# Kernel tuning notes

Hardware: AMD Instinct MI355X
Metric: run time of the kernel (lower is better)

Reference implementation:

```python
import jax, jax.numpy as jnp
import numpy as np

B, L = 8, 2048          # images, lines per image
C_IN, HW = 256, 128     # backbone feature channels, spatial size
DIM_LOI = 128
N_PTS0, N_PTS1 = 32, 8  # sampled points per line, after maxpool
SCALE = N_PTS0 // N_PTS1
EPS = 1e-5


def setup_inputs() -> dict:
    key = jax.random.key(0)
    ks = jax.random.split(key, 24)
    d = {}
    d['feature'] = jax.random.normal(ks[0], (B, C_IN, HW, HW), jnp.float32)
    # line endpoints in pixel coords [0, 128)
    d['lines'] = jax.random.uniform(ks[1], (B, L, 2, 2), jnp.float32) * HW
    # fc1: 1x1 conv 256 -> 128
    d['fc1_w'] = jax.random.normal(ks[2], (DIM_LOI, C_IN), jnp.float32) * 0.05
    d['fc1_b'] = jnp.zeros((DIM_LOI,), jnp.float32)
    planes = DIM_LOI // 2
    def bn(k, c):
        k1, k2, k3 = jax.random.split(k, 3)
        return (jax.random.normal(k1, (c,), jnp.float32) * 0.1 + 1.0,
                jax.random.normal(k2, (c,), jnp.float32) * 0.1,
                jax.random.normal(k3, (c,), jnp.float32) * 0.05,
                jax.random.uniform(jax.random.fold_in(k, 7), (c,), jnp.float32, 0.5, 1.5))
    d['bn1_g'], d['bn1_b'], d['bn1_m'], d['bn1_v'] = bn(ks[3], DIM_LOI)
    d['conv1_w'] = jax.random.normal(ks[4], (planes, DIM_LOI), jnp.float32) * 0.05
    d['conv1_b'] = jnp.zeros((planes,), jnp.float32)
    d['bn2_g'], d['bn2_b'], d['bn2_m'], d['bn2_v'] = bn(ks[5], planes)
    d['conv2_w'] = jax.random.normal(ks[6], (planes, planes, 3), jnp.float32) * 0.05
    d['conv2_b'] = jnp.zeros((planes,), jnp.float32)
    d['bn3_g'], d['bn3_b'], d['bn3_m'], d['bn3_v'] = bn(ks[7], planes)
    d['conv3_w'] = jax.random.normal(ks[8], (DIM_LOI, planes), jnp.float32) * 0.05
    d['conv3_b'] = jnp.zeros((DIM_LOI,), jnp.float32)
    d['fc2_w'] = jax.random.normal(ks[9], (1, DIM_LOI * N_PTS1), jnp.float32) * 0.02
    d['fc2_b'] = jnp.zeros((1,), jnp.float32)
    return d


def _bn(x, g, b, m, v):
    # x: [N, C, T], eval-mode batchnorm
    s = g * jax.lax.rsqrt(v + EPS)
    return x * s[None, :, None] + (b - m * s)[None, :, None]


def _loi_forward(feature, lines, fc1_w, fc1_b,
                 bn1_g, bn1_b, bn1_m, bn1_v, conv1_w, conv1_b,
                 bn2_g, bn2_b, bn2_m, bn2_v, conv2_w, conv2_b,
                 bn3_g, bn3_b, bn3_m, bn3_v, conv3_w, conv3_b,
                 fc2_w, fc2_b):
    # fc1: 1x1 conv -> [B, DIM_LOI, H, W]
    x = jnp.einsum('oc,bchw->bohw', fc1_w, feature) + fc1_b[None, :, None, None]

    # sample N_PTS0 points per line: p = p0*lam + p1*(1-lam) - 0.5
    lam = jnp.linspace(0.0, 1.0, N_PTS0, dtype=lines.dtype)  # [P]
    pts = (lines[:, :, 0, None, :] * lam[None, None, :, None]
           + lines[:, :, 1, None, :] * (1.0 - lam[None, None, :, None]) - 0.5)  # [B,L,P,2]
    px, py = pts[..., 0], pts[..., 1]
    px0 = jnp.clip(jnp.floor(px), 0.0, HW - 1.0)
    py0 = jnp.clip(jnp.floor(py), 0.0, HW - 1.0)
    px1 = jnp.clip(px0 + 1.0, 0.0, HW - 1.0)
    py1 = jnp.clip(py0 + 1.0, 0.0, HW - 1.0)
    px0l, py0l = px0.astype(jnp.int32), py0.astype(jnp.int32)
    px1l, py1l = px1.astype(jnp.int32), py1.astype(jnp.int32)

    def gather(f, ix, iy):  # f: [C,H,W], ix/iy: [L,P] -> [C,L,P]
        return f[:, ix, iy]

    gat = jax.vmap(gather)  # over batch
    xp = (gat(x, px0l, py0l) * ((px1 - px) * (py1 - py))[:, None]
          + gat(x, px1l, py0l) * ((px - px0) * (py1 - py))[:, None]
          + gat(x, px0l, py1l) * ((px1 - px) * (py - py0))[:, None]
          + gat(x, px1l, py1l) * ((px - px0) * (py - py0))[:, None])  # [B,C,L,P]

    xp = xp.transpose(0, 2, 1, 3).reshape(B * L, DIM_LOI, N_PTS0)  # [N,C,P]
    # MaxPool1d(kernel=stride=SCALE)
    xp = xp.reshape(B * L, DIM_LOI, N_PTS1, SCALE).max(axis=-1)  # [N,C,T=8]

    # Bottleneck1D residual: x + op(x)
    h = jax.nn.relu(_bn(xp, bn1_g, bn1_b, bn1_m, bn1_v))
    h = jnp.einsum('oc,nct->not', conv1_w, h) + conv1_b[None, :, None]
    h = jax.nn.relu(_bn(h, bn2_g, bn2_b, bn2_m, bn2_v))
    h = jax.lax.conv_general_dilated(h, conv2_w, (1,), [(1, 1)],
                                     dimension_numbers=('NCH', 'OIH', 'NCH'))
    h = h + conv2_b[None, :, None]
    h = jax.nn.relu(_bn(h, bn3_g, bn3_b, bn3_m, bn3_v))
    h = jnp.einsum('oc,nct->not', conv3_w, h) + conv3_b[None, :, None]
    xp = xp + h

    # fc2: ReLU -> Linear(dim_loi*n_pts1, 1)
    flat = jax.nn.relu(xp).reshape(B * L, DIM_LOI * N_PTS1)
    logits = (flat @ fc2_w.T + fc2_b).reshape(-1)  # [B*L]
    return logits


def reference(feature, lines, fc1_w, fc1_b,
              bn1_g, bn1_b, bn1_m, bn1_v, conv1_w, conv1_b,
              bn2_g, bn2_b, bn2_m, bn2_v, conv2_w, conv2_b,
              bn3_g, bn3_b, bn3_m, bn3_v, conv3_w, conv3_b,
              fc2_w, fc2_b):
    return _loi_forward(feature, lines, fc1_w, fc1_b,
                        bn1_g, bn1_b, bn1_m, bn1_v, conv1_w, conv1_b,
                        bn2_g, bn2_b, bn2_m, bn2_v, conv2_w, conv2_b,
                        bn3_g, bn3_b, bn3_m, bn3_v, conv3_w, conv3_b,
                        fc2_w, fc2_b)
```

## Files before the change

### kernel.cpp

```cpp
#include <hip/hip_runtime.h>

#define EPSBN 1e-5f

typedef _Float16 f16;
typedef _Float16 f16x8 __attribute__((ext_vector_type(8)));
typedef _Float16 f16x4 __attribute__((ext_vector_type(4)));
typedef _Float16 f16x2 __attribute__((ext_vector_type(2)));
typedef float    f32x4 __attribute__((ext_vector_type(4)));

__device__ inline unsigned int pack2(float a, float b) {
    union { f16x2 h; unsigned int u; } cv;
    cv.h[0] = (f16)a; cv.h[1] = (f16)b;
    return cv.u;
}
__device__ inline f16x4 hmax4(f16x4 a, f16x4 b) {
    f16x4 r;
    #pragma unroll
    for (int i = 0; i < 4; ++i) r[i] = a[i] > b[i] ? a[i] : b[i];
    return r;
}
__device__ inline f16x8 relu8(f16x8 v) {
    f16x8 r;
    #pragma unroll
    for (int i = 0; i < 8; ++i) r[i] = v[i] > (f16)0.f ? v[i] : (f16)0.f;
    return r;
}

__global__ void wprep_kernel(const float* __restrict__ fc1w,
                             const float* __restrict__ w1,
                             const float* __restrict__ w2,
                             const float* __restrict__ w3,
                             f16* __restrict__ dst) {
    const int i = blockIdx.x * 256 + threadIdx.x;
    float v;
    if (i < 32768)      v = fc1w[i];
    else if (i < 40960) v = w1[i - 32768];
    else if (i < 53248) {
        const int j = i - 40960, tau = j >> 12, rest = j & 4095;
        v = w2[rest * 3 + tau];
    } else              v = w3[i - 53248];
    dst[i] = (f16)v;
}

__global__ __launch_bounds__(256, 4)
void fc1_mfma(const float* __restrict__ feat,
              const f16*   __restrict__ w16,
              const float* __restrict__ bias,
              f16*         __restrict__ xmap) {
    __shared__ unsigned int ldsu[64 * 130];

    const int tid  = threadIdx.x;
    const int wv   = tid >> 6, lane = tid & 63;
    const int n16  = lane & 15, quad = lane >> 4;
    const int b    = blockIdx.x & 7;
    const int p0   = (blockIdx.x >> 3) * 64;
    const int lane16 = tid & 15;
    const int r2     = tid >> 4;

    const float* fbase = feat + ((size_t)b << 22) + p0 + lane16 * 4;
    #pragma unroll
    for (int i = 0; i < 8; ++i) {
        const int kp = r2 + 16 * i;
        const float* ra = fbase + ((size_t)(2 * kp) << 14);
        const float4 f4a = *(const float4*)ra;
        const float4 f4b = *(const float4*)(ra + 16384);
        ldsu[(lane16 * 4 + 0) * 130 + kp] = pack2(f4a.x, f4b.x);
        ldsu[(lane16 * 4 + 1) * 130 + kp] = pack2(f4a.y, f4b.y);
        ldsu[(lane16 * 4 + 2) * 130 + kp] = pack2(f4a.z, f4b.z);
        ldsu[(lane16 * 4 + 3) * 130 + kp] = pack2(f4a.w, f4b.w);
    }
    __syncthreads();

    f32x4 acc[8];
    #pragma unroll
    for (int nt = 0; nt < 8; ++nt) acc[nt] = (f32x4){0.f, 0.f, 0.f, 0.f};

    const unsigned int* arow = ldsu + (wv * 16 + n16) * 130;
    #pragma unroll
    for (int ks = 0; ks < 8; ++ks) {
        const int c = ks * 16 + quad * 4;
        union { f16x8 v; f16x4 h[2]; } af;
        af.h[0] = *(const f16x4*)&arow[c];
        af.h[1] = *(const f16x4*)&arow[c + 2];
        #pragma unroll
        for (int nt = 0; nt < 8; ++nt) {
            const f16x8 bf = *(const f16x8*)&w16[(size_t)(nt * 16 + n16) * 256
                                                 + ks * 32 + quad * 8];
            acc[nt] = __builtin_amdgcn_mfma_f32_16x16x32_f16(af.v, bf, acc[nt], 0, 0, 0);
        }
    }
    __syncthreads();

    f16* ep = (f16*)ldsu;
    #pragma unroll
    for (int nt = 0; nt < 8; ++nt) {
        const int o = nt * 16 + n16;
        const float bo = bias[o];
        #pragma unroll
        for (int r = 0; r < 4; ++r)
            ep[(wv * 16 + quad * 4 + r) * 136 + o] = (f16)(acc[nt][r] + bo);
    }
    __syncthreads();

    #pragma unroll
    for (int it = 0; it < 4; ++it) {
        const int u = tid + 256 * it;
        const int row = u >> 4, cg = u & 15;
        const float4 v = *(const float4*)&ep[row * 136 + cg * 8];
        *(float4*)&xmap[(((size_t)((b << 14) + p0 + row)) << 7) + cg * 8] = v;
    }
}

__global__ __launch_bounds__(256)
void loi_kernel(const f16*   __restrict__ x,
                const float* __restrict__ lines,
                const f16*   __restrict__ wsp,
                const float* __restrict__ bn1g, const float* __restrict__ bn1b,
                const float* __restrict__ bn1m, const float* __restrict__ bn1v,
                const float* __restrict__ b1,
                const float* __restrict__ bn2g, const float* __restrict__ bn2b,
                const float* __restrict__ bn2m, const float* __restrict__ bn2v,
                const float* __restrict__ b2,
                const float* __restrict__ bn3g, const float* __restrict__ bn3b,
                const float* __restrict__ bn3m, const float* __restrict__ bn3v,
                const float* __restrict__ b3,
                const float* __restrict__ fc2w, const float* __restrict__ fc2b,
                float* __restrict__ out) {
    __shared__ f16 xp[64][136];
    __shared__ alignas(16) union {
        struct { int toff[256][4]; f16 twgt[256][4]; } tp;
        struct { f16 h1[80][72]; f16 h2[64][72]; } cv;
    } u;
    __shared__ f16 s1h[128], t1h[128];
    __shared__ float s2f[64], t2f[64], s3f[64], t3f[64], b1f[64], b2f[64];
    __shared__ float b3f[128];
    __shared__ float wsum[4][8];

    const f16* w1f16 = wsp + 32768;
    const f16* w2f16 = wsp + 40960;
    const f16* w3f16 = wsp + 53248;

    const int tid  = threadIdx.x;
    const int wv   = tid >> 6, lane = tid & 63;
    const int n16  = lane & 15, quad = lane >> 4;
    const int img  = blockIdx.x & 7;
    const int mblk = blockIdx.x >> 3;

    if (tid < 128) {
        const float s = bn1g[tid] * rsqrtf(bn1v[tid] + EPSBN);
        s1h[tid] = (f16)s; t1h[tid] = (f16)(bn1b[tid] - bn1m[tid] * s);
    }
    if (tid < 64) {
        const float s = bn2g[tid] * rsqrtf(bn2v[tid] + EPSBN);
        s2f[tid] = s; t2f[tid] = bn2b[tid] - bn2m[tid] * s;
        b1f[tid] = b1[tid];
    } else if (tid < 128) {
        const int c = tid - 64;
        const float s = bn3g[c] * rsqrtf(bn3v[c] + EPSBN);
        s3f[c] = s; t3f[c] = bn3b[c] - bn3m[c] * s;
        b2f[c] = b2[c];
    } else {
        b3f[tid - 128] = b3[tid - 128];
    }

    {
        const int li = tid >> 5, pt = tid & 31;
        const int gl = img * 2048 + mblk * 8 + li;
        const float4 ln = *(const float4*)&lines[gl * 4];
        const float lam = (float)pt * (1.0f / 31.0f);
        const float px = ln.x * lam + ln.z * (1.f - lam) - 0.5f;
        const float py = ln.y * lam + ln.w * (1.f - lam) - 0.5f;
        const float px0 = fminf(fmaxf(floorf(px), 0.f), 127.f);
        const float py0 = fminf(fmaxf(floorf(py), 0.f), 127.f);
        const float px1 = fminf(px0 + 1.f, 127.f);
        const float py1 = fminf(py0 + 1.f, 127.f);
        const int ix0 = (int)px0, iy0 = (int)py0;
        const int ix1 = (int)px1, iy1 = (int)py1;
        u.tp.toff[tid][0] = (((ix0 << 7) + iy0) << 7);
        u.tp.toff[tid][1] = (((ix1 << 7) + iy0) << 7);
        u.tp.toff[tid][2] = (((ix0 << 7) + iy1) << 7);
        u.tp.toff[tid][3] = (((ix1 << 7) + iy1) << 7);
        const float wx1 = px1 - px, wx0 = px - px0;
        const float wy1 = py1 - py, wy0 = py - py0;
        u.tp.twgt[tid][0] = (f16)(wx1 * wy1); u.tp.twgt[tid][1] = (f16)(wx0 * wy1);
        u.tp.twgt[tid][2] = (f16)(wx1 * wy0); u.tp.twgt[tid][3] = (f16)(wx0 * wy0);
    }
    __syncthreads();

    {
        const int h = lane >> 5, j = lane & 31;
        const int li = wv * 2 + h;
        const f16* xbh = x + (((size_t)img) << 21) + 4 * j;
        #pragma unroll
        for (int t = 0; t < 8; ++t) {
            f16x4 m = {(f16)(-60000.f), (f16)(-60000.f), (f16)(-60000.f), (f16)(-60000.f)};
            #pragma unroll
            for (int s = 0; s < 4; ++s) {
                const int combo = li * 32 + t * 4 + s;
                const int4  off = *(const int4*)&u.tp.toff[combo][0];
                const f16x4 tw  = *(const f16x4*)&u.tp.twgt[combo][0];
                const f16x4 g00 = *(const f16x4*)(xbh + off.x);
                const f16x4 g10 = *(const f16x4*)(xbh + off.y);
                const f16x4 g01 = *(const f16x4*)(xbh + off.z);
                const f16x4 g11 = *(const f16x4*)(xbh + off.w);
                const f16x4 w0 = {tw[0], tw[0], tw[0], tw[0]};
                const f16x4 w1v = {tw[1], tw[1], tw[1], tw[1]};
                const f16x4 w2v = {tw[2], tw[2], tw[2], tw[2]};
                const f16x4 w3v = {tw[3], tw[3], tw[3], tw[3]};
                f16x4 v = g00 * w0 + g10 * w1v + g01 * w2v + g11 * w3v;
                m = hmax4(m, v);
            }
            *(f16x4*)&xp[li * 8 + t][4 * j] = m;
        }
    }
    __syncthreads();

    {
        const int r = tid >> 4, seg = tid & 15;
        const int row = (r >> 1) * 10 + (r & 1) * 9;
        *(unsigned long long*)&u.cv.h1[row][seg * 4] = 0ull;
    }

    {
        const int o_lane = wv * 16 + n16;
        f32x4 acc1[4];
        #pragma unroll
        for (int nt = 0; nt < 4; ++nt) acc1[nt] = (f32x4){0.f, 0.f, 0.f, 0.f};
        #pragma unroll
        for (int ks = 0; ks < 4; ++ks) {
            const int k = ks * 32 + quad * 8;
            const f16x8 a  = *(const f16x8*)&w1f16[o_lane * 128 + k];
            const f16x8 s8 = *(const f16x8*)&s1h[k];
            const f16x8 t8 = *(const f16x8*)&t1h[k];
            #pragma unroll
            for (int nt = 0; nt < 4; ++nt) {
                const f16x8 raw = *(const f16x8*)&xp[nt * 16 + n16][k];
                const f16x8 bf = relu8(raw * s8 + t8);
                acc1[nt] = __builtin_amdgcn_mfma_f32_16x16x32_f16(a, bf, acc1[nt], 0, 0, 0);
            }
        }
        #pragma unroll
        for (int nt = 0; nt < 4; ++nt) {
            const int n = nt * 16 + n16;
            const int nprow = (n >> 3) * 10 + (n & 7) + 1;
            #pragma unroll
            for (int r = 0; r < 4; ++r) {
                const int o = wv * 16 + quad * 4 + r;
                const float v = fmaxf((acc1[nt][r] + b1f[o]) * s2f[o] + t2f[o], 0.f);
                u.cv.h1[nprow][o] = (f16)v;
            }
        }
    }
    __syncthreads();

    {
        const int o_lane = wv * 16 + n16;
        f32x4 acc2[4];
        #pragma unroll
        for (int nt = 0; nt < 4; ++nt) acc2[nt] = (f32x4){0.f, 0.f, 0.f, 0.f};
        #pragma unroll
        for (int d = 0; d < 3; ++d) {
            const f16* A2 = w2f16 + d * 4096;
            #pragma unroll
            for (int ks = 0; ks < 2; ++ks) {
                const int k = ks * 32 + quad * 8;
                const f16x8 a = *(const f16x8*)&A2[o_lane * 64 + k];
                #pragma unroll
                for (int nt = 0; nt < 4; ++nt) {
                    const int n = nt * 16 + n16;
                    const int row = (n >> 3) * 10 + (n & 7) + d;
                    const f16x8 bf = *(const f16x8*)&u.cv.h1[row][k];
                    acc2[nt] = __builtin_amdgcn_mfma_f32_16x16x32_f16(a, bf, acc2[nt], 0, 0, 0);
                }
            }
        }
        #pragma unroll
        for (int nt = 0; nt < 4; ++nt) {
            const int n = nt * 16 + n16;
            #pragma unroll
            for (int r = 0; r < 4; ++r) {
                const int o = wv * 16 + quad * 4 + r;
                const float v = fmaxf((acc2[nt][r] + b2f[o]) * s3f[o] + t3f[o], 0.f);
                u.cv.h2[n][o] = (f16)v;
            }
        }
    }
    __syncthreads();

    {
        const int col = n16 & 7, obase = wv * 16 + quad * 4;
        float fcv[2][4];
        #pragma unroll
        for (int h = 0; h < 2; ++h)
            #pragma unroll
            for (int r = 0; r < 4; ++r)
                fcv[h][r] = fc2w[(h * 64 + obase + r) * 8 + col];

        f32x4 acc3[2][4];
        #pragma unroll
        for (int h = 0; h < 2; ++h)
            #pragma unroll
            for (int nt = 0; nt < 4; ++nt) acc3[h][nt] = (f32x4){0.f, 0.f, 0.f, 0.f};
        #pragma unroll
        for (int ks = 0; ks < 2; ++ks) {
            const int k = ks * 32 + quad * 8;
            const f16x8 a0 = *(const f16x8*)&w3f16[(wv * 16 + n16) * 64 + k];
            const f16x8 a1 = *(const f16x8*)&w3f16[(64 + wv * 16 + n16) * 64 + k];
            #pragma unroll
            for (int nt = 0; nt < 4; ++nt) {
                const f16x8 bf = *(const f16x8*)&u.cv.h2[nt * 16 + n16][k];
                acc3[0][nt] = __builtin_amdgcn_mfma_f32_16x16x32_f16(a0, bf, acc3[0][nt], 0, 0, 0);
                acc3[1][nt] = __builtin_amdgcn_mfma_f32_16x16x32_f16(a1, bf, acc3[1][nt], 0, 0, 0);
            }
        }
        float part[4] = {0.f, 0.f, 0.f, 0.f};
        #pragma unroll
        for (int h = 0; h < 2; ++h) {
            const float4 bq = *(const float4*)&b3f[h * 64 + obase];
            const float bqa[4] = {bq.x, bq.y, bq.z, bq.w};
            #pragma unroll
            for (int nt = 0; nt < 4; ++nt) {
                const int n = nt * 16 + n16;
                const f16x4 rx = *(const f16x4*)&xp[n][h * 64 + obase];
                float p = 0.f;
                #pragma unroll
                for (int r = 0; r < 4; ++r) {
                    float v = acc3[h][nt][r] + bqa[r] + (float)rx[r];
                    v = fmaxf(v, 0.f);
                    p += v * fcv[h][r];
                }
                part[nt] += p;
            }
        }
        #pragma unroll
        for (int off_i = 0; off_i < 5; ++off_i) {
            const int off = (int[]){1, 2, 4, 16, 32}[off_i];
            part[0] += __shfl_xor(part[0], off, 64);
            part[1] += __shfl_xor(part[1], off, 64);
            part[2] += __shfl_xor(part[2], off, 64);
            part[3] += __shfl_xor(part[3], off, 64);
        }
        if ((lane & 55) == 0) {
            const int par = (lane >> 3) & 1;
            wsum[wv][0 + par] = part[0];
            wsum[wv][2 + par] = part[1];
            wsum[wv][4 + par] = part[2];
            wsum[wv][6 + par] = part[3];
        }
    }
    __syncthreads();

    if (tid < 8) {
        const float s = wsum[0][tid] + wsum[1][tid] + wsum[2][tid] + wsum[3][tid];
        out[img * 2048 + mblk * 8 + tid] = s + fc2b[0];
    }
}

extern "C" void kernel_launch(void* const* d_in, const int* in_sizes, int n_in,
                              void* d_out, int out_size, void* d_ws, size_t ws_size,
                              hipStream_t stream) {
    const float* feature = (const float*)d_in[0];
    const float* lines   = (const float*)d_in[1];
    const float* fc1_w   = (const float*)d_in[2];
    const float* fc1_b   = (const float*)d_in[3];
    const float* bn1g    = (const float*)d_in[4];
    const float* bn1b    = (const float*)d_in[5];
    const float* bn1m    = (const float*)d_in[6];
    const float* bn1v    = (const float*)d_in[7];
    const float* w1      = (const float*)d_in[8];
    const float* b1      = (const float*)d_in[9];
    const float* bn2g    = (const float*)d_in[10];
    const float* bn2b    = (const float*)d_in[11];
    const float* bn2m    = (const float*)d_in[12];
    const float* bn2v    = (const float*)d_in[13];
    const float* w2      = (const float*)d_in[14];
    const float* b2      = (const float*)d_in[15];
    const float* bn3g    = (const float*)d_in[16];
    const float* bn3b    = (const float*)d_in[17];
    const float* bn3m    = (const float*)d_in[18];
    const float* bn3v    = (const float*)d_in[19];
    const float* w3      = (const float*)d_in[20];
    const float* b3      = (const float*)d_in[21];
    const float* fc2w    = (const float*)d_in[22];
    const float* fc2b    = (const float*)d_in[23];

    f16* xmap = (f16*)d_ws;
    f16* wsp  = (f16*)((char*)d_ws + (size_t)32 * 1024 * 1024);

    wprep_kernel<<<240, 256, 0, stream>>>(fc1_w, w1, w2, w3, wsp);
    fc1_mfma<<<2048, 256, 0, stream>>>(feature, wsp, fc1_b, xmap);
    loi_kernel<<<2048, 256, 0, stream>>>(xmap, lines, wsp,
                                         bn1g, bn1b, bn1m, bn1v, b1,
                                         bn2g, bn2b, bn2m, bn2v, b2,
                                         bn3g, bn3b, bn3m, bn3v, b3,
                                         fc2w, fc2b, (float*)d_out);
}
```

Measured before the change: 340.2 us.

## Split fc1 into fp16 transpose pass and tiled MFMA GEMM, chunked by image pairs

Replaces the fused fc1 kernel, which read fp32 NCHW features and transposed them in LDS, with two kernels. The first converts features to a pixel-major fp16 layout. The second is a 128x128-tile MFMA GEMM with register prefetch of the next K chunk. Work runs in four chunks of two images so the intermediate stays small and may stay cache-resident. This adds an extra write and read of the transposed features and eight more launches, in exchange for coalesced loads and more reuse of the weights.

Result: slower. 362.0 us (+6.4%).

```diff
diff --git a/kernel.cpp b/kernel.cpp
--- a/kernel.cpp
+++ b/kernel.cpp
@@ -8,11 +8,6 @@
 typedef _Float16 f16x2 __attribute__((ext_vector_type(2)));
 typedef float    f32x4 __attribute__((ext_vector_type(4)));
 
-__device__ inline unsigned int pack2(float a, float b) {
-    union { f16x2 h; unsigned int u; } cv;
-    cv.h[0] = (f16)a; cv.h[1] = (f16)b;
-    return cv.u;
-}
 __device__ inline f16x4 hmax4(f16x4 a, f16x4 b) {
     f16x4 r;
     #pragma unroll
@@ -42,72 +37,119 @@
     dst[i] = (f16)v;
 }
 
-__global__ __launch_bounds__(256, 4)
-void fc1_mfma(const float* __restrict__ feat,
-              const f16*   __restrict__ w16,
-              const float* __restrict__ bias,
-              f16*         __restrict__ xmap) {
-    __shared__ unsigned int ldsu[64 * 130];
+__global__ __launch_bounds__(256)
+void transpose_kernel(const float* __restrict__ feat,
+                      f16* __restrict__ featT,
+                      int b0) {
+    __shared__ float lds[64][129];
+
+    const int tid = threadIdx.x, wv = tid >> 6, lane = tid & 63;
+    const int bq  = blockIdx.x & 1;
+    const int kc  = (blockIdx.x >> 1) & 3;
+    const int p0  = (blockIdx.x >> 3) * 128;
+    const int k0  = kc * 64;
+
+    const float* src = feat + ((size_t)(b0 + bq) << 22) + (size_t)k0 * 16384 + p0;
+
+    #pragma unroll
+    for (int j = 0; j < 8; ++j) {
+        const int row = wv * 16 + 2 * j + (lane >> 5);
+        const int col = (lane & 31) * 4;
+        const float4 v = *(const float4*)(src + (size_t)row * 16384 + col);
+        *(float4*)&lds[row][col] = v;
+    }
+    __syncthreads();
+
+    const int a = lane >> 3, b = lane & 7;
+    #pragma unroll
+    for (int it = 0; it < 4; ++it) {
+        const int p = 8 * wv + a + 32 * it;
+        f16x8 h;
+        #pragma unroll
+        for (int j = 0; j < 8; ++j) h[j] = (f16)lds[b * 8 + j][p];
+        *(f16x8*)&featT[(((size_t)bq << 14) + p0 + p) * 256 + k0 + b * 8] = h;
+    }
+}
+
+__global__ __launch_bounds__(256)
+void gemm_kernel(const f16*   __restrict__ featT,
+                 const f16*   __restrict__ w16,
+                 const float* __restrict__ bias,
+                 f16*         __restrict__ xmap,
+                 int b0) {
+    __shared__ union {
+        f16 A[128][72];
+        f16 E[128][136];
+    } u;
 
     const int tid  = threadIdx.x;
     const int wv   = tid >> 6, lane = tid & 63;
     const int n16  = lane & 15, quad = lane >> 4;
-    const int b    = blockIdx.x & 7;
-    const int p0   = (blockIdx.x >> 3) * 64;
-    const int lane16 = tid & 15;
-    const int r2     = tid >> 4;
-
-    const float* fbase = feat + ((size_t)b << 22) + p0 + lane16 * 4;
-    #pragma unroll
-    for (int i = 0; i < 8; ++i) {
-        const int kp = r2 + 16 * i;
-        const float* ra = fbase + ((size_t)(2 * kp) << 14);
-        const float4 f4a = *(const float4*)ra;
-        const float4 f4b = *(const float4*)(ra + 16384);
-        ldsu[(lane16 * 4 + 0) * 130 + kp] = pack2(f4a.x, f4b.x);
-        ldsu[(lane16 * 4 + 1) * 130 + kp] = pack2(f4a.y, f4b.y);
-        ldsu[(lane16 * 4 + 2) * 130 + kp] = pack2(f4a.z, f4b.z);
-        ldsu[(lane16 * 4 + 3) * 130 + kp] = pack2(f4a.w, f4b.w);
-    }
-    __syncthreads();
-
-    f32x4 acc[8];
-    #pragma unroll
-    for (int nt = 0; nt < 8; ++nt) acc[nt] = (f32x4){0.f, 0.f, 0.f, 0.f};
-
-    const unsigned int* arow = ldsu + (wv * 16 + n16) * 130;
-    #pragma unroll
-    for (int ks = 0; ks < 8; ++ks) {
-        const int c = ks * 16 + quad * 4;
-        union { f16x8 v; f16x4 h[2]; } af;
-        af.h[0] = *(const f16x4*)&arow[c];
-        af.h[1] = *(const f16x4*)&arow[c + 2];
+    const int bq   = blockIdx.x & 1;
+    const int p0   = (blockIdx.x >> 1) * 128;
+    const int seg  = lane & 7;
+    const int rowb = wv * 8 + (lane >> 3);
+
+    const f16* src = featT + (((size_t)bq << 14) + p0) * 256;
+
+    f32x4 acc[2][8];
+    #pragma unroll
+    for (int mt = 0; mt < 2; ++mt)
+        #pragma unroll
+        for (int nt = 0; nt < 8; ++nt) acc[mt][nt] = (f32x4){0.f, 0.f, 0.f, 0.f};
+
+    f16x8 pf[4];
+    #pragma unroll
+    for (int it = 0; it < 4; ++it)
+        pf[it] = *(const f16x8*)(src + (size_t)(rowb + 32 * it) * 256 + seg * 8);
+
+    for (int kc = 0; kc < 4; ++kc) {
+        #pragma unroll
+        for (int it = 0; it < 4; ++it)
+            *(f16x8*)&u.A[rowb + 32 * it][seg * 8] = pf[it];
+        __syncthreads();
+        if (kc < 3) {
+            #pragma unroll
+            for (int it = 0; it < 4; ++it)
+                pf[it] = *(const f16x8*)(src + (size_t)(rowb + 32 * it) * 256
+                                         + (kc + 1) * 64 + seg * 8);
+        }
+        #pragma unroll
+        for (int s = 0; s < 2; ++s) {
+            const int kl = s * 32 + quad * 8;
+            const f16x8 a0 = *(const f16x8*)&u.A[(2 * wv + 0) * 16 + n16][kl];
+            const f16x8 a1 = *(const f16x8*)&u.A[(2 * wv + 1) * 16 + n16][kl];
+            #pragma unroll
+            for (int nt = 0; nt < 8; ++nt) {
+                const f16x8 bf = *(const f16x8*)&w16[(size_t)(nt * 16 + n16) * 256
+                                                     + kc * 64 + kl];
+                acc[0][nt] = __builtin_amdgcn_mfma_f32_16x16x32_f16(a0, bf, acc[0][nt], 0, 0, 0);
+                acc[1][nt] = __builtin_amdgcn_mfma_f32_16x16x32_f16(a1, bf, acc[1][nt], 0, 0, 0);
+            }
+        }
+        __syncthreads();
+    }
+
+    #pragma unroll
+    for (int mt = 0; mt < 2; ++mt) {
         #pragma unroll
         for (int nt = 0; nt < 8; ++nt) {
-            const f16x8 bf = *(const f16x8*)&w16[(size_t)(nt * 16 + n16) * 256
-                                                 + ks * 32 + quad * 8];
-            acc[nt] = __builtin_amdgcn_mfma_f32_16x16x32_f16(af.v, bf, acc[nt], 0, 0, 0);
-        }
-    }
-    __syncthreads();
-
-    f16* ep = (f16*)ldsu;
-    #pragma unroll
-    for (int nt = 0; nt < 8; ++nt) {
-        const int o = nt * 16 + n16;
-        const float bo = bias[o];
-        #pragma unroll
-        for (int r = 0; r < 4; ++r)
-            ep[(wv * 16 + quad * 4 + r) * 136 + o] = (f16)(acc[nt][r] + bo);
-    }
-    __syncthreads();
-
-    #pragma unroll
-    for (int it = 0; it < 4; ++it) {
-        const int u = tid + 256 * it;
-        const int row = u >> 4, cg = u & 15;
-        const float4 v = *(const float4*)&ep[row * 136 + cg * 8];
-        *(float4*)&xmap[(((size_t)((b << 14) + p0 + row)) << 7) + cg * 8] = v;
+            const int o = nt * 16 + n16;
+            const float bo = bias[o];
+            #pragma unroll
+            for (int r = 0; r < 4; ++r)
+                u.E[(2 * wv + mt) * 16 + quad * 4 + r][o] = (f16)(acc[mt][nt][r] + bo);
+        }
+    }
+    __syncthreads();
+
+    const int bglob = b0 + bq;
+    #pragma unroll
+    for (int it = 0; it < 8; ++it) {
+        const int uu = tid + 256 * it;
+        const int row = uu >> 4, cg = uu & 15;
+        const float4 v = *(const float4*)&u.E[row][cg * 8];
+        *(float4*)&xmap[(((size_t)((bglob << 14) + p0 + row)) << 7) + cg * 8] = v;
     }
 }
 
@@ -384,11 +426,17 @@
     const float* fc2w    = (const float*)d_in[22];
     const float* fc2b    = (const float*)d_in[23];
 
-    f16* xmap = (f16*)d_ws;
-    f16* wsp  = (f16*)((char*)d_ws + (size_t)32 * 1024 * 1024);
+    f16* wsp   = (f16*)d_ws;
+    f16* xmap  = (f16*)((char*)d_ws + (size_t)131072);
+    f16* featT = (f16*)((char*)d_ws + (size_t)131072 + (size_t)32 * 1024 * 1024);
 
     wprep_kernel<<<240, 256, 0, stream>>>(fc1_w, w1, w2, w3, wsp);
-    fc1_mfma<<<2048, 256, 0, stream>>>(feature, wsp, fc1_b, xmap);
+
+    for (int b0 = 0; b0 < 8; b0 += 2) {
+        transpose_kernel<<<1024, 256, 0, stream>>>(feature, featT, b0);
+        gemm_kernel<<<256, 256, 0, stream>>>(featT, wsp, fc1_b, xmap, b0);
+    }
+
     loi_kernel<<<2048, 256, 0, stream>>>(xmap, lines, wsp,
                                          bn1g, bn1b, bn1m, bn1v, b1,
                                          bn2g, bn2b, bn2m, bn2v, b2,
```

## Pipeline fc1 feature loads in K-chunks with register prefetch and smaller LDS

Applied to the files above, without the earlier changes.

The fc1 GEMM kernel now streams the 256 input channels in four chunks of 64. It stages fp32 tiles in a smaller LDS buffer and prefetches the next chunk into registers while MFMAs run on the current one, instead of loading all channels up front as packed fp16. This is meant to overlap global loads with compute and cut LDS footprint for higher occupancy. The fp16 conversion moves to the LDS read side, and the launch-bounds occupancy hint is dropped. The workspace layout is also swapped so the weights come first and xmap follows at a small offset.

New measurement: 355.8 us. +4.6%, slower.

```diff
diff --git a/kernel.cpp b/kernel.cpp
--- a/kernel.cpp
+++ b/kernel.cpp
@@ -8,11 +8,6 @@
 typedef _Float16 f16x2 __attribute__((ext_vector_type(2)));
 typedef float    f32x4 __attribute__((ext_vector_type(4)));
 
-__device__ inline unsigned int pack2(float a, float b) {
-    union { f16x2 h; unsigned int u; } cv;
-    cv.h[0] = (f16)a; cv.h[1] = (f16)b;
-    return cv.u;
-}
 __device__ inline f16x4 hmax4(f16x4 a, f16x4 b) {
     f16x4 r;
     #pragma unroll
@@ -42,71 +37,80 @@
     dst[i] = (f16)v;
 }
 
-__global__ __launch_bounds__(256, 4)
+__global__ __launch_bounds__(256)
 void fc1_mfma(const float* __restrict__ feat,
               const f16*   __restrict__ w16,
               const float* __restrict__ bias,
               f16*         __restrict__ xmap) {
-    __shared__ unsigned int ldsu[64 * 130];
+    __shared__ union {
+        float A[64][66];
+        f16   E[64][136];
+    } u;
 
     const int tid  = threadIdx.x;
     const int wv   = tid >> 6, lane = tid & 63;
     const int n16  = lane & 15, quad = lane >> 4;
     const int b    = blockIdx.x & 7;
     const int p0   = (blockIdx.x >> 3) * 64;
-    const int lane16 = tid & 15;
-    const int r2     = tid >> 4;
-
-    const float* fbase = feat + ((size_t)b << 22) + p0 + lane16 * 4;
-    #pragma unroll
-    for (int i = 0; i < 8; ++i) {
-        const int kp = r2 + 16 * i;
-        const float* ra = fbase + ((size_t)(2 * kp) << 14);
-        const float4 f4a = *(const float4*)ra;
-        const float4 f4b = *(const float4*)(ra + 16384);
-        ldsu[(lane16 * 4 + 0) * 130 + kp] = pack2(f4a.x, f4b.x);
-        ldsu[(lane16 * 4 + 1) * 130 + kp] = pack2(f4a.y, f4b.y);
-        ldsu[(lane16 * 4 + 2) * 130 + kp] = pack2(f4a.z, f4b.z);
-        ldsu[(lane16 * 4 + 3) * 130 + kp] = pack2(f4a.w, f4b.w);
-    }
-    __syncthreads();
+    const int krow = tid >> 4;
+    const int pcol = (tid & 15) * 4;
+
+    const float* src = feat + ((size_t)b << 22) + p0 + pcol;
 
     f32x4 acc[8];
     #pragma unroll
     for (int nt = 0; nt < 8; ++nt) acc[nt] = (f32x4){0.f, 0.f, 0.f, 0.f};
 
-    const unsigned int* arow = ldsu + (wv * 16 + n16) * 130;
-    #pragma unroll
-    for (int ks = 0; ks < 8; ++ks) {
-        const int c = ks * 16 + quad * 4;
-        union { f16x8 v; f16x4 h[2]; } af;
-        af.h[0] = *(const f16x4*)&arow[c];
-        af.h[1] = *(const f16x4*)&arow[c + 2];
-        #pragma unroll
-        for (int nt = 0; nt < 8; ++nt) {
-            const f16x8 bf = *(const f16x8*)&w16[(size_t)(nt * 16 + n16) * 256
-                                                 + ks * 32 + quad * 8];
-            acc[nt] = __builtin_amdgcn_mfma_f32_16x16x32_f16(af.v, bf, acc[nt], 0, 0, 0);
-        }
-    }
-    __syncthreads();
-
-    f16* ep = (f16*)ldsu;
+    float4 pf[4];
+    #pragma unroll
+    for (int i = 0; i < 4; ++i)
+        pf[i] = *(const float4*)(src + ((size_t)(krow + 16 * i) << 14));
+
+    for (int kc = 0; kc < 4; ++kc) {
+        #pragma unroll
+        for (int i = 0; i < 4; ++i)
+            *(float4*)&u.A[krow + 16 * i][pcol] = pf[i];
+        __syncthreads();
+
+        if (kc < 3) {
+            #pragma unroll
+            for (int i = 0; i < 4; ++i)
+                pf[i] = *(const float4*)(src + ((size_t)((kc + 1) * 64 + krow + 16 * i) << 14));
+        }
+
+        #pragma unroll
+        for (int ks = 0; ks < 2; ++ks) {
+            const int kb = ks * 32 + quad * 8;
+            const int pm = wv * 16 + n16;
+            f16x8 af;
+            #pragma unroll
+            for (int j = 0; j < 8; ++j)
+                af[j] = (f16)u.A[kb + j][pm];
+            #pragma unroll
+            for (int nt = 0; nt < 8; ++nt) {
+                const f16x8 bf = *(const f16x8*)&w16[(size_t)(nt * 16 + n16) * 256
+                                                     + kc * 64 + kb];
+                acc[nt] = __builtin_amdgcn_mfma_f32_16x16x32_f16(af, bf, acc[nt], 0, 0, 0);
+            }
+        }
+        __syncthreads();
+    }
+
     #pragma unroll
     for (int nt = 0; nt < 8; ++nt) {
         const int o = nt * 16 + n16;
         const float bo = bias[o];
         #pragma unroll
         for (int r = 0; r < 4; ++r)
-            ep[(wv * 16 + quad * 4 + r) * 136 + o] = (f16)(acc[nt][r] + bo);
+            u.E[wv * 16 + quad * 4 + r][o] = (f16)(acc[nt][r] + bo);
     }
     __syncthreads();
 
     #pragma unroll
     for (int it = 0; it < 4; ++it) {
-        const int u = tid + 256 * it;
-        const int row = u >> 4, cg = u & 15;
-        const float4 v = *(const float4*)&ep[row * 136 + cg * 8];
+        const int uu = tid + 256 * it;
+        const int row = uu >> 4, cg = uu & 15;
+        const float4 v = *(const float4*)&u.E[row][cg * 8];
         *(float4*)&xmap[(((size_t)((b << 14) + p0 + row)) << 7) + cg * 8] = v;
     }
 }
@@ -384,8 +388,8 @@
     const float* fc2w    = (const float*)d_in[22];
     const float* fc2b    = (const float*)d_in[23];
 
-    f16* xmap = (f16*)d_ws;
-    f16* wsp  = (f16*)((char*)d_ws + (size_t)32 * 1024 * 1024);
+    f16* wsp  = (f16*)d_ws;
+    f16* xmap = (f16*)((char*)d_ws + (size_t)131072);
 
     wprep_kernel<<<240, 256, 0, stream>>>(fc1_w, w1, w2, w3, wsp);
     fc1_mfma<<<2048, 256, 0, stream>>>(feature, wsp, fc1_b, xmap);
```
